# Kernel optimization log

Hardware: AMD Instinct MI355X
Metric: run time of the kernel (lower is better)

Reference implementation:

```python
import jax, jax.numpy as jnp
from jax import lax
import numpy as np

DEPTH = 6
DIM = 512            # embed_dim
DI = 768             # d_inner = int(1.5 * 512)
B = 64
IMG = 224
P = 16               # patch size == stride
HW = 14              # patches per side
NP = HW * HW         # 196


def _ln(x, w, b, eps=1e-5):
    m = jnp.mean(x, axis=-1, keepdims=True)
    v = jnp.var(x, axis=-1, keepdims=True)
    return (x - m) / jnp.sqrt(v + eps) * w + b


def _mamba(x, in_w, out_w, cw, cb, dw, db, A, D):
    # x: (N, L, DIM); in_w: (2*DI, DIM); out_w: (DIM, DI); cw: (DI, 3)
    xz = jnp.einsum('nlc,dc->nld', x, in_w)          # (N, L, 2*DI)
    xi, z = jnp.split(xz, 2, axis=-1)
    # depthwise conv1d, kernel=3, padding=1
    xp = jnp.pad(xi, ((0, 0), (1, 1), (0, 0)))
    xc = xp[:, :-2] * cw[:, 0] + xp[:, 1:-1] * cw[:, 1] + xp[:, 2:] * cw[:, 2] + cb
    xc = jax.nn.silu(xc)
    dt = jax.nn.softplus(jnp.einsum('nld,ed->nle', xc, dw) + db)
    Ae = jnp.exp(A * dt)                              # A < 0, dt > 0 -> stable
    y = jnp.cumsum(xc * dt * Ae, axis=1) * Ae + xc * D
    y = y * jax.nn.silu(z)
    return jnp.einsum('nld,cd->nlc', y, out_w)


def _forward(x, patch_w, patch_b, cls_token, pos_embed,
             blk_norm_w, blk_norm_b,
             mh_in_w, mh_out_w, mh_conv_w, mh_conv_b, mh_dt_w, mh_dt_b, mh_A, mh_D,
             mv_in_w, mv_out_w, mv_conv_w, mv_conv_b, mv_dt_w, mv_dt_b, mv_A, mv_D,
             fus_w, fus_b, ss_norm_w, ss_norm_b, fn_w, fn_b):
    Bsz = x.shape[0]
    # patch embed: Conv2d(3, DIM, k=16, s=16)
    feat = lax.conv_general_dilated(x, patch_w, window_strides=(P, P), padding='VALID',
                                    dimension_numbers=('NCHW', 'OIHW', 'NCHW'))
    feat = feat + patch_b[None, :, None, None]
    feat = feat.reshape(Bsz, DIM, NP).transpose(0, 2, 1)  # (B, 196, DIM)
    tok = jnp.concatenate([jnp.broadcast_to(cls_token, (Bsz, 1, DIM)), feat], axis=1)
    tok = tok + pos_embed                                  # (B, 197, DIM)
    for i in range(DEPTH):
        cls = tok[:, :1]
        pt = tok[:, 1:]
        pn = _ln(pt, blk_norm_w[i], blk_norm_b[i])
        p2 = pn.reshape(Bsz, HW, HW, DIM)
        # horizontal scan: rows as sequences
        yh = _mamba(p2.reshape(Bsz * HW, HW, DIM),
                    mh_in_w[i], mh_out_w[i], mh_conv_w[i], mh_conv_b[i],
                    mh_dt_w[i], mh_dt_b[i], mh_A[i], mh_D[i]).reshape(Bsz, HW, HW, DIM)
        # vertical scan: columns as sequences
        xv = p2.transpose(0, 2, 1, 3).reshape(Bsz * HW, HW, DIM)
        yv = _mamba(xv,
                    mv_in_w[i], mv_out_w[i], mv_conv_w[i], mv_conv_b[i],
                    mv_dt_w[i], mv_dt_b[i], mv_A[i], mv_D[i])
        yv = yv.reshape(Bsz, HW, HW, DIM).transpose(0, 2, 1, 3)
        yc = jnp.concatenate([yh, yv], axis=-1)            # (B, H, W, 2*DIM)
        yf = jnp.einsum('bhwk,ck->bhwc', yc, fus_w[i]) + fus_b[i]
        p_out = _ln(yf + p2, ss_norm_w[i], ss_norm_b[i]).reshape(Bsz, NP, DIM)
        cls_out = cls + _ln(cls, blk_norm_w[i], blk_norm_b[i])
        tok = jnp.concatenate([cls_out, p_out], axis=1)
    return _ln(tok, fn_w, fn_b)


def setup_inputs() -> dict:
    key = jax.random.key(0)
    ks = jax.random.split(key, 32)
    s = 0.02
    d = {}
    d['x'] = jax.random.normal(ks[0], (B, 3, IMG, IMG), jnp.float32)
    d['patch_w'] = jax.random.normal(ks[1], (DIM, 3, P, P), jnp.float32) * s
    d['patch_b'] = jnp.zeros((DIM,), jnp.float32)
    d['cls_token'] = jax.random.normal(ks[2], (1, 1, DIM), jnp.float32) * s
    d['pos_embed'] = jax.random.normal(ks[3], (1, NP + 1, DIM), jnp.float32) * s
    d['blk_norm_w'] = jnp.ones((DEPTH, DIM), jnp.float32)
    d['blk_norm_b'] = jnp.zeros((DEPTH, DIM), jnp.float32)
    for pfx, base in (('mh', 4), ('mv', 12)):
        d[pfx + '_in_w'] = jax.random.normal(ks[base + 0], (DEPTH, 2 * DI, DIM), jnp.float32) * s
        d[pfx + '_out_w'] = jax.random.normal(ks[base + 1], (DEPTH, DIM, DI), jnp.float32) * s
        d[pfx + '_conv_w'] = jax.random.normal(ks[base + 2], (DEPTH, DI, 3), jnp.float32) * 0.2
        d[pfx + '_conv_b'] = jnp.zeros((DEPTH, DI), jnp.float32)
        d[pfx + '_dt_w'] = jax.random.normal(ks[base + 3], (DEPTH, DI, DI), jnp.float32) * s
        d[pfx + '_dt_b'] = jnp.zeros((DEPTH, DI), jnp.float32)
        d[pfx + '_A'] = -jax.random.uniform(ks[base + 4], (DEPTH, DI), jnp.float32) * 0.1
        d[pfx + '_D'] = jnp.ones((DEPTH, DI), jnp.float32)
    d['fus_w'] = jax.random.normal(ks[20], (DEPTH, DIM, 2 * DIM), jnp.float32) * s
    d['fus_b'] = jnp.zeros((DEPTH, DIM), jnp.float32)
    d['ss_norm_w'] = jnp.ones((DEPTH, DIM), jnp.float32)
    d['ss_norm_b'] = jnp.zeros((DEPTH, DIM), jnp.float32)
    d['fn_w'] = jnp.ones((DIM,), jnp.float32)
    d['fn_b'] = jnp.zeros((DIM,), jnp.float32)
    return d


def reference(x, patch_w, patch_b, cls_token, pos_embed,
              blk_norm_w, blk_norm_b,
              mh_in_w, mh_out_w, mh_conv_w, mh_conv_b, mh_dt_w, mh_dt_b, mh_A, mh_D,
              mv_in_w, mv_out_w, mv_conv_w, mv_conv_b, mv_dt_w, mv_dt_b, mv_A, mv_D,
              fus_w, fus_b, ss_norm_w, ss_norm_b, fn_w, fn_b):
    return _forward(x, patch_w, patch_b, cls_token, pos_embed,
                    blk_norm_w, blk_norm_b,
                    mh_in_w, mh_out_w, mh_conv_w, mh_conv_b, mh_dt_w, mh_dt_b, mh_A, mh_D,
                    mv_in_w, mv_out_w, mv_conv_w, mv_conv_b, mv_dt_w, mv_dt_b, mv_A, mv_D,
                    fus_w, fus_b, ss_norm_w, ss_norm_b, fn_w, fn_b)
```

## Files before the change

kernel.cpp:

```cpp
#include <hip/hip_runtime.h>
#include <cstdint>


using u16 = unsigned short;
typedef __attribute__((ext_vector_type(8))) short   bfrag;
typedef __attribute__((ext_vector_type(4))) float   ffrag;
typedef __attribute__((ext_vector_type(8))) u16     u16x8;

__device__ __forceinline__ float b2f(u16 u) {
  union { float f; uint32_t i; } c; c.i = ((uint32_t)u) << 16; return c.f;
}
__device__ __forceinline__ u16 f2b(float f) {
  union { float f; uint32_t i; } c; c.f = f;
  uint32_t r = c.i + 0x7FFFu + ((c.i >> 16) & 1u);
  return (u16)(r >> 16);
}

#define LOG2E 1.44269504f
#define LN2   0.69314718f
__device__ __forceinline__ float fexp(float x) {
  return __builtin_amdgcn_exp2f(x * LOG2E);
}
__device__ __forceinline__ float fsigmoid(float x) {
  return __builtin_amdgcn_rcpf(1.f + __builtin_amdgcn_exp2f(-x * LOG2E));
}
__device__ __forceinline__ float fsilu(float x) { return x * fsigmoid(x); }
__device__ __forceinline__ float fsoftplus(float x) {
  float e = __builtin_amdgcn_exp2f(-fabsf(x) * LOG2E);
  return fmaxf(x, 0.f) + LN2 * __builtin_amdgcn_logf(1.f + e);
}

__device__ __forceinline__ void gl_lds16(const u16* g, u16* l) {
  __builtin_amdgcn_global_load_lds(
      (const __attribute__((address_space(1))) void*)g,
      (__attribute__((address_space(3))) void*)l,
      16, 0, 0);
}

__global__ __launch_bounds__(256, 2)
void gemm_dual(const u16* __restrict__ A, const u16* __restrict__ W1,
               const u16* __restrict__ W2, u16* __restrict__ C,
               int K, int lda, int ldc, int nsplit, int acol2, int ccol2)
{
  __shared__ u16 As[128 * 64];
  __shared__ u16 Bs[128 * 64];

  const int total = gridDim.x * gridDim.y;
  const int flat  = blockIdx.y * gridDim.x + blockIdx.x;
  const int chunk = total >> 3;
  const int f2    = (flat & 7) * chunk + (flat >> 3);
  const int bx    = f2 % gridDim.x;
  const int by    = f2 / gridDim.x;

  const bool second = bx >= nsplit;
  const u16* W     = second ? W2 : W1;
  const int n0l    = (bx - (second ? nsplit : 0)) * 128;
  const int acol   = second ? acol2 : 0;
  const int ccol0  = n0l + (second ? ccol2 : 0);
  const int m0     = by * 128;

  const int tid  = threadIdx.x;
  const int lane = tid & 63;
  const int wv   = tid >> 6;
  const int wm   = wv >> 1;
  const int wn   = wv & 1;

  const int lr   = lane >> 3;
  const int lc   = lane & 7;
  const int kcol = (lc ^ lr) << 3;

  const size_t abase = (size_t)(m0 + wv * 32 + lr) * lda + acol + kcol;
  const size_t wbase = (size_t)(n0l + wv * 32 + lr) * K + kcol;

  const ffrag fz = {0.f, 0.f, 0.f, 0.f};
  ffrag acc[4][4];
#pragma unroll
  for (int i = 0; i < 4; ++i)
#pragma unroll
    for (int j = 0; j < 4; ++j) acc[i][j] = fz;

  const int fr = lane & 15;
  const int fq = lane >> 4;

  for (int kb = 0; kb < K; kb += 64) {
#pragma unroll
    for (int i = 0; i < 4; ++i)
      gl_lds16(A + abase + (size_t)(i * 8) * lda + kb, &As[(wv * 4 + i) * 512]);
#pragma unroll
    for (int i = 0; i < 4; ++i)
      gl_lds16(W + wbase + (size_t)(i * 8) * K + kb, &Bs[(wv * 4 + i) * 512]);
    __syncthreads();

#pragma unroll
    for (int ks = 0; ks < 2; ++ks) {
      bfrag af[4], bfr[4];
#pragma unroll
      for (int t = 0; t < 4; ++t) {
        int r  = wm * 64 + t * 16 + fr;
        int ca = ((ks * 4 + fq) ^ (r & 7)) << 3;
        af[t]  = *(const bfrag*)&As[r * 64 + ca];
        int n  = wn * 64 + t * 16 + fr;
        int cb = ((ks * 4 + fq) ^ (n & 7)) << 3;
        bfr[t] = *(const bfrag*)&Bs[n * 64 + cb];
      }
#pragma unroll
      for (int i = 0; i < 4; ++i)
#pragma unroll
        for (int j = 0; j < 4; ++j)
          acc[i][j] = __builtin_amdgcn_mfma_f32_16x16x32_bf16(
              af[i], bfr[j], acc[i][j], 0, 0, 0);
    }
    __syncthreads();
  }

#pragma unroll
  for (int i = 0; i < 4; ++i)
#pragma unroll
    for (int j = 0; j < 4; ++j)
#pragma unroll
      for (int rg = 0; rg < 4; ++rg) {
        int row = m0 + wm * 64 + i * 16 + fq * 4 + rg;
        int col = ccol0 + wn * 64 + j * 16 + fr;
        C[(size_t)row * ldc + col] = f2b(acc[i][j][rg]);
      }
}

__global__ __launch_bounds__(256, 2)
void gemm_wprep(const u16* __restrict__ WB, const u16* __restrict__ OT,
                u16* __restrict__ WF)
{
  __shared__ u16 As[128 * 64];
  __shared__ u16 Bs[128 * 64];

  const int z = blockIdx.z, L = z >> 1, path = z & 1;
  const u16* A = WB + (size_t)L * 4063232 + 3538944;
  const u16* W = OT + (size_t)z * 393216;
  u16* C = WF + (size_t)L * 786432;

  const int m0 = blockIdx.y * 128, n0l = blockIdx.x * 128;
  const int acol = path * 512, ccol = path * 768;

  const int tid  = threadIdx.x;
  const int lane = tid & 63;
  const int wv   = tid >> 6;
  const int wm   = wv >> 1;
  const int wn   = wv & 1;
  const int lr   = lane >> 3;
  const int lc   = lane & 7;
  const int kcol = (lc ^ lr) << 3;

  const size_t abase = (size_t)(m0 + wv * 32 + lr) * 1024 + acol + kcol;
  const size_t wbase = (size_t)(n0l + wv * 32 + lr) * 512 + kcol;

  const ffrag fz = {0.f, 0.f, 0.f, 0.f};
  ffrag acc[4][4];
#pragma unroll
  for (int i = 0; i < 4; ++i)
#pragma unroll
    for (int j = 0; j < 4; ++j) acc[i][j] = fz;

  const int fr = lane & 15;
  const int fq = lane >> 4;

  for (int kb = 0; kb < 512; kb += 64) {
#pragma unroll
    for (int i = 0; i < 4; ++i)
      gl_lds16(A + abase + (size_t)(i * 8) * 1024 + kb, &As[(wv * 4 + i) * 512]);
#pragma unroll
    for (int i = 0; i < 4; ++i)
      gl_lds16(W + wbase + (size_t)(i * 8) * 512 + kb, &Bs[(wv * 4 + i) * 512]);
    __syncthreads();

#pragma unroll
    for (int ks = 0; ks < 2; ++ks) {
      bfrag af[4], bfr[4];
#pragma unroll
      for (int t = 0; t < 4; ++t) {
        int r  = wm * 64 + t * 16 + fr;
        int ca = ((ks * 4 + fq) ^ (r & 7)) << 3;
        af[t]  = *(const bfrag*)&As[r * 64 + ca];
        int n  = wn * 64 + t * 16 + fr;
        int cb = ((ks * 4 + fq) ^ (n & 7)) << 3;
        bfr[t] = *(const bfrag*)&Bs[n * 64 + cb];
      }
#pragma unroll
      for (int i = 0; i < 4; ++i)
#pragma unroll
        for (int j = 0; j < 4; ++j)
          acc[i][j] = __builtin_amdgcn_mfma_f32_16x16x32_bf16(
              af[i], bfr[j], acc[i][j], 0, 0, 0);
    }
    __syncthreads();
  }

#pragma unroll
  for (int i = 0; i < 4; ++i)
#pragma unroll
    for (int j = 0; j < 4; ++j)
#pragma unroll
      for (int rg = 0; rg < 4; ++rg) {
        int row = m0 + wm * 64 + i * 16 + fq * 4 + rg;
        int col = ccol + n0l + wn * 64 + j * 16 + fr;
        C[(size_t)row * 1536 + col] = f2b(acc[i][j][rg]);
      }
}

__global__ __launch_bounds__(256)
void k_transp(const float* __restrict__ mho, const float* __restrict__ mvo,
              u16* __restrict__ OT)
{
  __shared__ float ld[32][33];
  const int z = blockIdx.z, L = z >> 1, path = z & 1;
  const float* src = (path ? mvo : mho) + (size_t)L * 393216;
  u16* dst = OT + (size_t)z * 393216;
  const int tx = threadIdx.x & 31, ty = threadIdx.x >> 5;
  const int dx = blockIdx.x * 32, cy = blockIdx.y * 32;
#pragma unroll
  for (int i = 0; i < 4; ++i)
    ld[ty + 8 * i][tx] = src[(size_t)(cy + ty + 8 * i) * 768 + dx + tx];
  __syncthreads();
#pragma unroll
  for (int i = 0; i < 4; ++i)
    dst[(size_t)(dx + ty + 8 * i) * 512 + cy + tx] = f2b(ld[tx][ty + 8 * i]);
}

__global__ __launch_bounds__(256)
void k_cvt_all(const float* __restrict__ mhi, const float* __restrict__ mhd,
               const float* __restrict__ mho, const float* __restrict__ mvi,
               const float* __restrict__ mvd, const float* __restrict__ mvo,
               const float* __restrict__ fus, u16* __restrict__ dst)
{
  size_t e = ((size_t)blockIdx.x * 256 + threadIdx.x) * 8;
  int L = (int)(e / 4063232);
  int r = (int)(e - (size_t)L * 4063232);
  const float* s; int off;
  if      (r <  786432) { s = mhi + (size_t)L *  786432; off = r; }
  else if (r < 1376256) { s = mhd + (size_t)L *  589824; off = r -  786432; }
  else if (r < 1769472) { s = mho + (size_t)L *  393216; off = r - 1376256; }
  else if (r < 2555904) { s = mvi + (size_t)L *  786432; off = r - 1769472; }
  else if (r < 3145728) { s = mvd + (size_t)L *  589824; off = r - 2555904; }
  else if (r < 3538944) { s = mvo + (size_t)L *  393216; off = r - 3145728; }
  else                  { s = fus + (size_t)L *  524288; off = r - 3538944; }
  float4 a = *(const float4*)(s + off);
  float4 b = *(const float4*)(s + off + 4);
  u16x8 o;
  o[0] = f2b(a.x); o[1] = f2b(a.y); o[2] = f2b(a.z); o[3] = f2b(a.w);
  o[4] = f2b(b.x); o[5] = f2b(b.y); o[6] = f2b(b.z); o[7] = f2b(b.w);
  *(u16x8*)(dst + e) = o;
}

__global__ __launch_bounds__(256)
void k_cvt1(const float* __restrict__ s, u16* __restrict__ dst)
{
  int e = (blockIdx.x * 256 + threadIdx.x) * 8;
  float4 a = *(const float4*)(s + e);
  float4 b = *(const float4*)(s + e + 4);
  u16x8 o;
  o[0] = f2b(a.x); o[1] = f2b(a.y); o[2] = f2b(a.z); o[3] = f2b(a.w);
  o[4] = f2b(b.x); o[5] = f2b(b.y); o[6] = f2b(b.z); o[7] = f2b(b.w);
  *(u16x8*)(dst + e) = o;
}

__global__ __launch_bounds__(256) void k_im2col(const float* __restrict__ x,
                                                u16* __restrict__ im)
{
  int idx = blockIdx.x * 256 + threadIdx.x;
  int r = idx % 96, p = idx / 96;
  int b = p / 196, q = p - b * 196;
  int ph = q / 14, pw = q - ph * 14;
  int k = r * 8;
  int c = k >> 8, k2 = k & 255;
  int i = k2 >> 4, j = k2 & 15;
  const float* src = x + (((size_t)(b * 3 + c) * 224 + ph * 16 + i) * 224
                          + pw * 16 + j);
  float4 a = *(const float4*)src;
  float4 d = *(const float4*)(src + 4);
  u16x8 o;
  o[0] = f2b(a.x); o[1] = f2b(a.y); o[2] = f2b(a.z); o[3] = f2b(a.w);
  o[4] = f2b(d.x); o[5] = f2b(d.y); o[6] = f2b(d.z); o[7] = f2b(d.w);
  *(u16x8*)(im + (size_t)p * 768 + k) = o;
}

__global__ __launch_bounds__(256)
void k_addbias_ln(u16* __restrict__ TOK, const float* __restrict__ pb,
                  const float* __restrict__ pos, const float* __restrict__ w,
                  const float* __restrict__ b)
{
  int row  = blockIdx.x * 4 + (threadIdx.x >> 6);
  int lane = threadIdx.x & 63;
  int base = lane * 8;
  int tpos = 1 + (row % 196);
  u16* p = TOK + (size_t)row * 512 + base;
  u16x8 t = *(u16x8*)p;
  const float* pv = pos + (size_t)tpos * 512 + base;
  float v[8]; float s = 0.f, qq = 0.f;
#pragma unroll
  for (int i = 0; i < 8; ++i) {
    v[i] = b2f(t[i]) + pb[base + i] + pv[i];
    s += v[i]; qq += v[i] * v[i];
  }
#pragma unroll
  for (int o = 32; o; o >>= 1) { s += __shfl_xor(s, o, 64); qq += __shfl_xor(qq, o, 64); }
  float mean = s * (1.f / 512.f);
  float rstd = rsqrtf(qq * (1.f / 512.f) - mean * mean + 1e-5f);
  u16x8 ov;
#pragma unroll
  for (int i = 0; i < 8; ++i)
    ov[i] = f2b((v[i] - mean) * rstd * w[base + i] + b[base + i]);
  *(u16x8*)p = ov;
}

__global__ __launch_bounds__(256) void k_ln_fuse(const u16* __restrict__ YF,
                                                 u16* __restrict__ TOK,
                                                 const float* __restrict__ fb,
                                                 const float* __restrict__ w,
                                                 const float* __restrict__ b)
{
  int row  = blockIdx.x * 4 + (threadIdx.x >> 6);
  int lane = threadIdx.x & 63;
  int base = lane * 8;
  const u16* yf = YF + (size_t)row * 512 + base;
  u16* tp = TOK + (size_t)row * 512 + base;
  u16x8 yv = *(const u16x8*)yf;
  u16x8 tv = *(u16x8*)tp;
  float v[8]; float s = 0.f, qq = 0.f;
#pragma unroll
  for (int i = 0; i < 8; ++i) {
    v[i] = b2f(yv[i]) + fb[base + i] + b2f(tv[i]);
    s += v[i]; qq += v[i] * v[i];
  }
#pragma unroll
  for (int o = 32; o; o >>= 1) { s += __shfl_xor(s, o, 64); qq += __shfl_xor(qq, o, 64); }
  float mean = s * (1.f / 512.f);
  float rstd = rsqrtf(qq * (1.f / 512.f) - mean * mean + 1e-5f);
  u16x8 ov;
#pragma unroll
  for (int i = 0; i < 8; ++i)
    ov[i] = f2b((v[i] - mean) * rstd * w[base + i] + b[base + i]);
  *(u16x8*)tp = ov;
}

__global__ __launch_bounds__(256)
void k_ln_fuse2(const u16* __restrict__ YF, u16* __restrict__ TOK,
                const float* __restrict__ fb, const float* __restrict__ w1,
                const float* __restrict__ b1, const float* __restrict__ w2,
                const float* __restrict__ b2)
{
  int row  = blockIdx.x * 4 + (threadIdx.x >> 6);
  int lane = threadIdx.x & 63;
  int base = lane * 8;
  const u16* yf = YF + (size_t)row * 512 + base;
  u16* tp = TOK + (size_t)row * 512 + base;
  u16x8 yv = *(const u16x8*)yf;
  u16x8 tv = *(u16x8*)tp;
  float v[8]; float s = 0.f, qq = 0.f;
#pragma unroll
  for (int i = 0; i < 8; ++i) {
    v[i] = b2f(yv[i]) + fb[base + i] + b2f(tv[i]);
    s += v[i]; qq += v[i] * v[i];
  }
#pragma unroll
  for (int o = 32; o; o >>= 1) { s += __shfl_xor(s, o, 64); qq += __shfl_xor(qq, o, 64); }
  float mean = s * (1.f / 512.f);
  float rstd = rsqrtf(qq * (1.f / 512.f) - mean * mean + 1e-5f);
  float s2 = 0.f, q2 = 0.f;
#pragma unroll
  for (int i = 0; i < 8; ++i) {
    v[i] = (v[i] - mean) * rstd * w1[base + i] + b1[base + i];
    s2 += v[i]; q2 += v[i] * v[i];
  }
#pragma unroll
  for (int o = 32; o; o >>= 1) { s2 += __shfl_xor(s2, o, 64); q2 += __shfl_xor(q2, o, 64); }
  float m2 = s2 * (1.f / 512.f);
  float r2 = rsqrtf(q2 * (1.f / 512.f) - m2 * m2 + 1e-5f);
  u16x8 ov;
#pragma unroll
  for (int i = 0; i < 8; ++i)
    ov[i] = f2b((v[i] - m2) * r2 * w2[base + i] + b2[base + i]);
  *(u16x8*)tp = ov;
}

__global__ __launch_bounds__(256)
void k_conv_hv(const u16* __restrict__ XZ,
               const float* __restrict__ cwh, const float* __restrict__ cbh,
               const float* __restrict__ cwv, const float* __restrict__ cbv,
               u16* __restrict__ XC)
{
  int idx = blockIdx.x * 256 + threadIdx.x;
  int half = idx >= 344064;
  int t = idx - (half ? 344064 : 0);
  int dp = t % 384, sq = t / 384;
  int d0 = dp * 2;
  int rowbase, rowstride;
  if (!half) { rowbase = sq * 14; rowstride = 1; }
  else       { int b = sq / 14, wq = sq - b * 14; rowbase = b * 196 + wq; rowstride = 14; }
  const float* cw = half ? cwv : cwh;
  const float* cb = half ? cbv : cbh;
  int xio = half ? 1536 : 0, xco = half ? 768 : 0;
  float w0a = cw[d0 * 3 + 0], w1a = cw[d0 * 3 + 1], w2a = cw[d0 * 3 + 2];
  float w0b = cw[d0 * 3 + 3], w1b = cw[d0 * 3 + 4], w2b = cw[d0 * 3 + 5];
  float ba = cb[d0], bb = cb[d0 + 1];
  uint32_t cu = *(const uint32_t*)&XZ[(size_t)rowbase * 3072 + xio + d0];
  float pa = 0.f, pb = 0.f;
  float ca = b2f((u16)cu), cbv2 = b2f((u16)(cu >> 16));
#pragma unroll
  for (int l = 0; l < 14; ++l) {
    int row = rowbase + l * rowstride;
    float na = 0.f, nb = 0.f;
    if (l < 13) {
      uint32_t nu = *(const uint32_t*)&XZ[(size_t)(row + rowstride) * 3072 + xio + d0];
      na = b2f((u16)nu); nb = b2f((u16)(nu >> 16));
    }
    float ua = pa * w0a + ca * w1a + na * w2a + ba;
    float ub = pb * w0b + cbv2 * w1b + nb * w2b + bb;
    uint32_t ov = (uint32_t)f2b(fsilu(ua)) | ((uint32_t)f2b(fsilu(ub)) << 16);
    *(uint32_t*)&XC[(size_t)row * 1536 + xco + d0] = ov;
    pa = ca; pb = cbv2; ca = na; cbv2 = nb;
  }
}

__global__ __launch_bounds__(256)
void k_scan_hv(const u16* __restrict__ XZ, u16* __restrict__ XC,
               const float* __restrict__ dtbh, const float* __restrict__ Ah,
               const float* __restrict__ Dh,
               const float* __restrict__ dtbv, const float* __restrict__ Av,
               const float* __restrict__ Dv)
{
  int idx = blockIdx.x * 256 + threadIdx.x;
  int half = idx >= 344064;
  int t = idx - (half ? 344064 : 0);
  int dp = t % 384, sq = t / 384;
  int d0 = dp * 2;
  int rowbase, rowstride;
  if (!half) { rowbase = sq * 14; rowstride = 1; }
  else       { int b = sq / 14, wq = sq - b * 14; rowbase = b * 196 + wq; rowstride = 14; }
  int xio = half ? 1536 : 0, xco = half ? 768 : 0;
  const float* dtb = half ? dtbv : dtbh;
  const float* Ap  = half ? Av : Ah;
  const float* Dp  = half ? Dv : Dh;
  float dba = dtb[d0], dbb = dtb[d0 + 1];
  float Aa = Ap[d0], Ab = Ap[d0 + 1];
  float Da = Dp[d0], Db = Dp[d0 + 1];
  float ra = 0.f, rb = 0.f;
#pragma unroll
  for (int l = 0; l < 14; ++l) {
    int row = rowbase + l * rowstride;
    size_t zb = (size_t)row * 3072 + xio;
    size_t cbo = (size_t)row * 1536 + xco;
    uint32_t xcu = *(const uint32_t*)&XC[cbo + d0];
    uint32_t dtu = *(const uint32_t*)&XZ[zb + d0];
    uint32_t zu  = *(const uint32_t*)&XZ[zb + 768 + d0];
    float xca = b2f((u16)xcu), xcb = b2f((u16)(xcu >> 16));
    float dta = fsoftplus(b2f((u16)dtu) + dba);
    float dtbv2 = fsoftplus(b2f((u16)(dtu >> 16)) + dbb);
    float aea = fexp(Aa * dta), aeb = fexp(Ab * dtbv2);
    ra += xca * dta * aea;
    rb += xcb * dtbv2 * aeb;
    float za = b2f((u16)zu), zbv = b2f((u16)(zu >> 16));
    float ya = (ra * aea + xca * Da) * (za * fsigmoid(za));
    float yb = (rb * aeb + xcb * Db) * (zbv * fsigmoid(zbv));
    *(uint32_t*)&XC[cbo + d0] = (uint32_t)f2b(ya) | ((uint32_t)f2b(yb) << 16);
  }
}

__global__ void k_cls(const float* __restrict__ cls_tok,
                      const float* __restrict__ pos,
                      const float* __restrict__ bw, const float* __restrict__ bb,
                      float* __restrict__ CLS)
{
  __shared__ float rs[8], rq[8], stat[2];
  int n = threadIdx.x;
  float v = cls_tok[n] + pos[n];
  for (int l = 0; l < 6; ++l) {
    float s = v, q = v * v;
#pragma unroll
    for (int o = 32; o; o >>= 1) { s += __shfl_xor(s, o, 64); q += __shfl_xor(q, o, 64); }
    if ((n & 63) == 0) { rs[n >> 6] = s; rq[n >> 6] = q; }
    __syncthreads();
    if (n == 0) {
      float S = 0.f, Q = 0.f;
      for (int i = 0; i < 8; ++i) { S += rs[i]; Q += rq[i]; }
      float m = S * (1.f / 512.f);
      stat[0] = m; stat[1] = rsqrtf(Q * (1.f / 512.f) - m * m + 1e-5f);
    }
    __syncthreads();
    float u = (v - stat[0]) * stat[1] * bw[l * 512 + n] + bb[l * 512 + n];
    v = v + u;
    __syncthreads();
  }
  CLS[n] = v;
}

__global__ __launch_bounds__(256) void k_final(const u16* __restrict__ TOK,
                                               const float* __restrict__ CLS,
                                               const float* __restrict__ w,
                                               const float* __restrict__ b,
                                               float* __restrict__ out)
{
  int row  = blockIdx.x * 4 + (threadIdx.x >> 6);
  int lane = threadIdx.x & 63;
  int bi = row / 197;
  int t  = row - bi * 197;
  int base = lane * 8;
  float v[8]; float s = 0.f, qq = 0.f;
  if (t == 0) {
#pragma unroll
    for (int i = 0; i < 8; ++i) v[i] = CLS[base + i];
  } else {
    const u16* src = TOK + ((size_t)bi * 196 + (t - 1)) * 512 + base;
    u16x8 tv = *(const u16x8*)src;
#pragma unroll
    for (int i = 0; i < 8; ++i) v[i] = b2f(tv[i]);
  }
#pragma unroll
  for (int i = 0; i < 8; ++i) { s += v[i]; qq += v[i] * v[i]; }
#pragma unroll
  for (int o = 32; o; o >>= 1) { s += __shfl_xor(s, o, 64); qq += __shfl_xor(qq, o, 64); }
  float mean = s * (1.f / 512.f);
  float rstd = rsqrtf(qq * (1.f / 512.f) - mean * mean + 1e-5f);
  float* op = out + (size_t)row * 512 + base;
#pragma unroll
  for (int i = 0; i < 8; ++i)
    op[i] = (v[i] - mean) * rstd * w[base + i] + b[base + i];
}

extern "C" void kernel_launch(void* const* d_in, const int* in_sizes, int n_in,
                              void* d_out, int out_size, void* d_ws, size_t ws_size,
                              hipStream_t stream)
{
  const float* x        = (const float*)d_in[0];
  const float* patch_w  = (const float*)d_in[1];
  const float* patch_b  = (const float*)d_in[2];
  const float* cls_tok  = (const float*)d_in[3];
  const float* pos      = (const float*)d_in[4];
  const float* blk_w    = (const float*)d_in[5];
  const float* blk_b    = (const float*)d_in[6];
  const float* mh_in_w  = (const float*)d_in[7];
  const float* mh_out_w = (const float*)d_in[8];
  const float* mh_cw    = (const float*)d_in[9];
  const float* mh_cb    = (const float*)d_in[10];
  const float* mh_dtw   = (const float*)d_in[11];
  const float* mh_dtb   = (const float*)d_in[12];
  const float* mh_A     = (const float*)d_in[13];
  const float* mh_D     = (const float*)d_in[14];
  const float* mv_in_w  = (const float*)d_in[15];
  const float* mv_out_w = (const float*)d_in[16];
  const float* mv_cw    = (const float*)d_in[17];
  const float* mv_cb    = (const float*)d_in[18];
  const float* mv_dtw   = (const float*)d_in[19];
  const float* mv_dtb   = (const float*)d_in[20];
  const float* mv_A     = (const float*)d_in[21];
  const float* mv_D     = (const float*)d_in[22];
  const float* fus_w    = (const float*)d_in[23];
  const float* fus_b    = (const float*)d_in[24];
  const float* ss_w     = (const float*)d_in[25];
  const float* ss_b     = (const float*)d_in[26];
  const float* fn_w     = (const float*)d_in[27];
  const float* fn_b     = (const float*)d_in[28];

  char* ws = (char*)d_ws;
  u16*   TOK  = (u16*)  (ws);
  u16*   XZHV = (u16*)  (ws +  12845056);
  u16*   XCHV = (u16*)  (ws +  89915392);
  u16*   WB   = (u16*)  (ws + 128450560);
  u16*   WP   = (u16*)  (ws + 177209344);
  u16*   OT   = (u16*)  (ws + 178782208);
  u16*   WF   = (u16*)  (ws + 188219392);
  float* CLS  = (float*)(ws + 197656576);
  u16*   IM   = XCHV;
  u16*   YF   = XZHV;

  const size_t LS = 4063232;
  const size_t oMHI = 0, oMHD = 786432, oMVI = 1769472, oMVD = 2555904;

  k_cvt_all<<<11904, 256, 0, stream>>>(mh_in_w, mh_dtw, mh_out_w,
                                       mv_in_w, mv_dtw, mv_out_w, fus_w, WB);
  k_transp<<<dim3(24, 16, 12), 256, 0, stream>>>(mh_out_w, mv_out_w, OT);
  gemm_wprep<<<dim3(6, 4, 12), 256, 0, stream>>>(WB, OT, WF);
  k_cvt1<<<192, 256, 0, stream>>>(patch_w, WP);
  k_im2col<<<4704, 256, 0, stream>>>(x, IM);
  gemm_dual<<<dim3(4, 98), 256, 0, stream>>>(IM, WP, WP, TOK,
                                             768, 768, 512, 4, 0, 0);
  k_addbias_ln<<<3136, 256, 0, stream>>>(TOK, patch_b, pos, blk_w, blk_b);
  k_cls<<<1, 512, 0, stream>>>(cls_tok, pos, blk_w, blk_b, CLS);

  for (int L = 0; L < 6; ++L) {
    const u16* wl = WB + (size_t)L * LS;

    gemm_dual<<<dim3(24, 98), 256, 0, stream>>>(
        TOK, wl + oMHI, wl + oMVI, XZHV, 512, 512, 3072, 12, 0, 1536);
    k_conv_hv<<<2688, 256, 0, stream>>>(XZHV, mh_cw + L * 2304, mh_cb + L * 768,
                                        mv_cw + L * 2304, mv_cb + L * 768, XCHV);
    gemm_dual<<<dim3(12, 98), 256, 0, stream>>>(
        XCHV, wl + oMHD, wl + oMVD, XZHV, 768, 1536, 3072, 6, 768, 1536);
    k_scan_hv<<<2688, 256, 0, stream>>>(XZHV, XCHV,
                                        mh_dtb + L * 768, mh_A + L * 768, mh_D + L * 768,
                                        mv_dtb + L * 768, mv_A + L * 768, mv_D + L * 768);
    gemm_dual<<<dim3(4, 98), 256, 0, stream>>>(
        XCHV, WF + (size_t)L * 786432, WF + (size_t)L * 786432, YF,
        1536, 1536, 512, 4, 0, 0);
    if (L < 5) {
      k_ln_fuse2<<<3136, 256, 0, stream>>>(YF, TOK, fus_b + L * 512,
                                           ss_w + L * 512, ss_b + L * 512,
                                           blk_w + (L + 1) * 512, blk_b + (L + 1) * 512);
    } else {
      k_ln_fuse<<<3136, 256, 0, stream>>>(YF, TOK, fus_b + L * 512,
                                          ss_w + L * 512, ss_b + L * 512);
    }
  }

  k_final<<<3152, 256, 0, stream>>>(TOK, CLS, fn_w, fn_b, (float*)d_out);
  (void)in_sizes; (void)n_in; (void)out_size; (void)ws_size;
}
```

Measured before the change: 1.239 ms.

## Add 256x256-tile 8-wave GEMM with staged LDS pipeline for in-proj and dt-proj

Adds a new bf16 MFMA GEMM that computes 256x256 output tiles with 512 threads, a 128KB LDS buffer split into half-K slots, and prefetch of A/B half-tiles interleaved with MFMA phases under barriers and s_setprio. It also uses an XCD remap that handles a block count not divisible by 8. The two per-layer projection GEMMs (in_proj and dt_proj) now use it instead of the 128x128 kernel. The aim is more data reuse per LDS load and better overlap of global loads with compute. The cost is higher register and LDS pressure and fewer workgroups (588 and 294), which risks poor occupancy and tail imbalance across CUs.

```diff
diff --git a/kernel.cpp b/kernel.cpp
--- a/kernel.cpp
+++ b/kernel.cpp
@@ -35,6 +35,166 @@
       (const __attribute__((address_space(1))) void*)g,
       (__attribute__((address_space(3))) void*)l,
       16, 0, 0);
+}
+
+__global__ __launch_bounds__(512, 2)
+void gemm_256(const u16* __restrict__ A, const u16* __restrict__ W1,
+              const u16* __restrict__ W2, u16* __restrict__ C,
+              int K, int lda, int ldc, int nsplit, int acol2, int ccol2)
+{
+  __shared__ u16 lds[65536];
+
+  const int nwg  = gridDim.x * gridDim.y;
+  const int flat = blockIdx.y * gridDim.x + blockIdx.x;
+  const int q8 = nwg >> 3, r8 = nwg & 7;
+  const int xcd = flat & 7, sidx = flat >> 3;
+  const int f2 = (xcd < r8 ? xcd * (q8 + 1)
+                           : r8 * (q8 + 1) + (xcd - r8) * q8) + sidx;
+  const int bx = f2 % gridDim.x;
+  const int by = f2 / gridDim.x;
+
+  const bool second = bx >= nsplit;
+  const u16* W    = second ? W2 : W1;
+  const int n0l   = (bx - (second ? nsplit : 0)) * 256;
+  const int acol  = second ? acol2 : 0;
+  const int ccol0 = n0l + (second ? ccol2 : 0);
+  const int m0    = by * 256;
+
+  const int tid  = threadIdx.x;
+  const int lane = tid & 63;
+  const int w    = tid >> 6;
+  const int wm   = w >> 2;
+  const int wn   = w & 3;
+
+  const int jj0 = (w * 2 + 0) * 8 + (lane >> 3);
+  const int jj1 = (w * 2 + 1) * 8 + (lane >> 3);
+  const int cc  = lane & 7;
+  const int ch0 = cc ^ (jj0 & 7);
+  const int ch1 = cc ^ (jj1 & 7);
+  const int r0 = 2 * jj0 + (ch0 >> 2), fq0 = ch0 & 3;
+  const int r1 = 2 * jj1 + (ch1 >> 2), fq1 = ch1 & 3;
+  const uint32_t aoff0 = (uint32_t)(m0 + r0) * lda + acol + fq0 * 8;
+  const uint32_t aoff1 = (uint32_t)(m0 + r1) * lda + acol + fq1 * 8;
+  const uint32_t boff0 = (uint32_t)(n0l + r0) * K + fq0 * 8;
+  const uint32_t boff1 = (uint32_t)(n0l + r1) * K + fq1 * 8;
+  u16* ldss0 = &lds[(w * 2 + 0) * 512];
+  u16* ldss1 = &lds[(w * 2 + 1) * 512];
+
+  auto STAGE_A = [&](int kk, int slot) {
+    gl_lds16(A + aoff0 + kk, ldss0 + slot * 8192);
+    gl_lds16(A + aoff1 + kk, ldss1 + slot * 8192);
+  };
+  auto STAGE_B = [&](int kk, int slot) {
+    gl_lds16(W + boff0 + kk, ldss0 + slot * 8192);
+    gl_lds16(W + boff1 + kk, ldss1 + slot * 8192);
+  };
+
+  const int fr  = lane & 15;
+  const int fqc = lane >> 4;
+  const int j0a = wm * 64 + (fr >> 1);
+  const int j0b = wn * 32 + (fr >> 1);
+  const int offA = j0a * 128 + (((((fr & 1) << 2) | fqc) ^ (j0a & 7)) << 4);
+  const int offB = j0b * 128 + (((((fr & 1) << 2) | fqc) ^ (j0b & 7)) << 4);
+  const char* ldsc = (const char*)lds;
+
+  const ffrag fz = {0.f, 0.f, 0.f, 0.f};
+  ffrag acc[8][4];
+#pragma unroll
+  for (int i = 0; i < 8; ++i)
+#pragma unroll
+    for (int j = 0; j < 4; ++j) acc[i][j] = fz;
+
+  const int NT = K >> 6;
+
+  STAGE_A(0, 0);  STAGE_B(0, 1);  STAGE_A(32, 2);  STAGE_B(32, 3);
+  STAGE_A(64, 4); STAGE_B(64, 5); STAGE_A(96, 6);
+  asm volatile("s_waitcnt vmcnt(6)" ::: "memory");
+  __builtin_amdgcn_s_barrier();
+
+  bfrag a0[8], a1[8], b0[4], b1[4];
+  for (int T = 0; T < NT; ++T) {
+    const int sb = (T & 1) << 2;
+    const int so = sb ^ 4;
+    const char* pA0 = ldsc + (sb + 0) * 16384;
+    const char* pB0 = ldsc + (sb + 1) * 16384;
+    const char* pA1 = ldsc + (sb + 2) * 16384;
+    const char* pB1 = ldsc + (sb + 3) * 16384;
+
+#pragma unroll
+    for (int t = 0; t < 8; ++t)
+      a0[t] = *(const bfrag*)(pA0 + offA + t * 1024);
+#pragma unroll
+    for (int c = 0; c < 4; ++c)
+      b0[c] = *(const bfrag*)(pB0 + offB + c * 1024);
+    if (T + 1 < NT) STAGE_B((T + 1) * 64 + 32, so + 3);
+    __builtin_amdgcn_s_barrier();
+    __builtin_amdgcn_s_setprio(1);
+#pragma unroll
+    for (int i = 0; i < 4; ++i)
+#pragma unroll
+      for (int j = 0; j < 4; ++j)
+        acc[i][j] = __builtin_amdgcn_mfma_f32_16x16x32_bf16(
+            a0[i], b0[j], acc[i][j], 0, 0, 0);
+    __builtin_amdgcn_s_setprio(0);
+    __builtin_amdgcn_s_barrier();
+
+#pragma unroll
+    for (int t = 0; t < 8; ++t)
+      a1[t] = *(const bfrag*)(pA1 + offA + t * 1024);
+    if (T + 2 < NT) STAGE_A((T + 2) * 64, sb + 0);
+    __builtin_amdgcn_s_barrier();
+    __builtin_amdgcn_s_setprio(1);
+#pragma unroll
+    for (int i = 0; i < 4; ++i)
+#pragma unroll
+      for (int j = 0; j < 4; ++j)
+        acc[4 + i][j] = __builtin_amdgcn_mfma_f32_16x16x32_bf16(
+            a0[4 + i], b0[j], acc[4 + i][j], 0, 0, 0);
+    __builtin_amdgcn_s_setprio(0);
+    __builtin_amdgcn_s_barrier();
+
+#pragma unroll
+    for (int c = 0; c < 4; ++c)
+      b1[c] = *(const bfrag*)(pB1 + offB + c * 1024);
+    if (T + 2 < NT) STAGE_B((T + 2) * 64, sb + 1);
+    __builtin_amdgcn_s_barrier();
+    __builtin_amdgcn_s_setprio(1);
+#pragma unroll
+    for (int i = 0; i < 4; ++i)
+#pragma unroll
+      for (int j = 0; j < 4; ++j)
+        acc[i][j] = __builtin_amdgcn_mfma_f32_16x16x32_bf16(
+            a1[i], b1[j], acc[i][j], 0, 0, 0);
+    __builtin_amdgcn_s_setprio(0);
+    __builtin_amdgcn_s_barrier();
+
+    if (T + 2 < NT) STAGE_A((T + 2) * 64 + 32, sb + 2);
+    __builtin_amdgcn_s_barrier();
+    __builtin_amdgcn_s_setprio(1);
+#pragma unroll
+    for (int i = 0; i < 4; ++i)
+#pragma unroll
+      for (int j = 0; j < 4; ++j)
+        acc[4 + i][j] = __builtin_amdgcn_mfma_f32_16x16x32_bf16(
+            a1[4 + i], b1[j], acc[4 + i][j], 0, 0, 0);
+    __builtin_amdgcn_s_setprio(0);
+    if (T + 2 < NT)
+      asm volatile("s_waitcnt vmcnt(6)" ::: "memory");
+    else if (T + 2 == NT)
+      asm volatile("s_waitcnt vmcnt(0)" ::: "memory");
+    __builtin_amdgcn_s_barrier();
+  }
+
+#pragma unroll
+  for (int i = 0; i < 8; ++i)
+#pragma unroll
+    for (int j = 0; j < 4; ++j)
+#pragma unroll
+      for (int rg = 0; rg < 4; ++rg) {
+        int row = m0 + wm * 128 + i * 16 + fqc * 4 + rg;
+        int col = ccol0 + wn * 64 + j * 16 + fr;
+        C[(size_t)row * ldc + col] = f2b(acc[i][j][rg]);
+      }
 }
 
 __global__ __launch_bounds__(256, 2)
@@ -587,12 +747,12 @@
   for (int L = 0; L < 6; ++L) {
     const u16* wl = WB + (size_t)L * LS;
 
-    gemm_dual<<<dim3(24, 98), 256, 0, stream>>>(
-        TOK, wl + oMHI, wl + oMVI, XZHV, 512, 512, 3072, 12, 0, 1536);
+    gemm_256<<<dim3(12, 49), 512, 0, stream>>>(
+        TOK, wl + oMHI, wl + oMVI, XZHV, 512, 512, 3072, 6, 0, 1536);
     k_conv_hv<<<2688, 256, 0, stream>>>(XZHV, mh_cw + L * 2304, mh_cb + L * 768,
                                         mv_cw + L * 2304, mv_cb + L * 768, XCHV);
-    gemm_dual<<<dim3(12, 98), 256, 0, stream>>>(
-        XCHV, wl + oMHD, wl + oMVD, XZHV, 768, 1536, 3072, 6, 768, 1536);
+    gemm_256<<<dim3(6, 49), 512, 0, stream>>>(
+        XCHV, wl + oMHD, wl + oMVD, XZHV, 768, 1536, 3072, 3, 768, 1536);
     k_scan_hv<<<2688, 256, 0, stream>>>(XZHV, XCHV,
                                         mh_dtb + L * 768, mh_A + L * 768, mh_D + L * 768,
                                         mv_dtb + L * 768, mv_A + L * 768, mv_D + L * 768);
```

Measured after the change: 1.403 ms. +13.2%, slower.
